# Kernel optimization log

Hardware: AMD Instinct MI355X
Metric: run time of the kernel (lower is better)

The kernel has to match this reference:

```python
import jax, jax.numpy as jnp
import numpy as np

EPS = 1e-5  # BatchNorm2d default eps


def _conv3x3(x, w):
    # x: [B,C,H,W], w: [O,I,3,3], stride 1, padding 1, no bias
    return jax.lax.conv_general_dilated(
        x, w, window_strides=(1, 1), padding=((1, 1), (1, 1)),
        dimension_numbers=("NCHW", "OIHW", "NCHW"))


def setup_inputs() -> dict:
    key = jax.random.key(0)
    k1, k2, k3 = jax.random.split(key, 3)
    B, C, H, W = 4, 64, 24, 24
    x = jax.random.normal(k1, (B, C, H, W), dtype=jnp.float32)
    gamma = jnp.ones((C,), dtype=jnp.float32)
    beta = jnp.zeros((C,), dtype=jnp.float32)
    # fan-based init scale as in the custom Conv2d (scale=1 and scale=1e-6)
    fan_qkv = (C + 3 * C) / 2 * 9
    bound_qkv = np.sqrt(3.0 / fan_qkv)
    w_qkv = jax.random.uniform(k2, (3 * C, C, 3, 3), minval=-bound_qkv,
                               maxval=bound_qkv, dtype=jnp.float32)
    fan_out = (C + C) / 2 * 9
    bound_out = np.sqrt(3.0 * 1e-6 / fan_out)
    w_out = jax.random.uniform(k3, (C, C, 3, 3), minval=-bound_out,
                               maxval=bound_out, dtype=jnp.float32)
    return {"x": x, "gamma": gamma, "beta": beta, "w_qkv": w_qkv, "w_out": w_out}


def reference(x, gamma, beta, w_qkv, w_out):
    B, C, H, W = x.shape
    # BatchNorm2d (training-mode batch statistics, biased variance)
    mean = jnp.mean(x, axis=(0, 2, 3), keepdims=True)
    var = jnp.var(x, axis=(0, 2, 3), keepdims=True)
    xn = (x - mean) * jax.lax.rsqrt(var + EPS)
    xn = xn * gamma[None, :, None, None] + beta[None, :, None, None]
    qkv = _conv3x3(xn, w_qkv)            # [B,3C,H,W]
    q, k, v = jnp.split(qkv, 3, axis=1)  # each [B,C,H,W]
    scale = 1.0 / np.sqrt(C)
    # per-channel attention: head_dim=1, heads=C
    logits = jnp.einsum("bcyx,bchw->bcyxhw", q, k) * scale  # [B,C,H,W,H,W]
    attn = jax.nn.softmax(logits.reshape(B, C, H, W, H * W), axis=-1)
    attn = attn.reshape(B, C, H, W, H, W)
    out_v = jnp.einsum("bcyxhw,bchw->bcyx", attn, v)  # [B,C,H,W]
    return x + _conv3x3(out_v, w_out)
```

## Files before the change

kernel.cpp:

```cpp
#include <hip/hip_runtime.h>
#include <math.h>

#define B_SZ 4
#define C_IN 64
#define HW_ 576
#define PPLANE 728
#define XH_N   (B_SZ * 32 * PPLANE)
#define WQH_N  (192 * 32 * 9)
#define WOH_N  (64 * 32 * 9)

typedef _Float16 h2 __attribute__((ext_vector_type(2)));
typedef _Float16 h4 __attribute__((ext_vector_type(4)));
typedef _Float16 h8 __attribute__((ext_vector_type(8)));

static __device__ __forceinline__ h2 lo2(h4 v) { return __builtin_shufflevector(v, v, 0, 1); }
static __device__ __forceinline__ h2 hi2(h4 v) { return __builtin_shufflevector(v, v, 2, 3); }

static __device__ __forceinline__ float dot2(h2 a, h2 b, float c) {
#if __has_builtin(__builtin_amdgcn_fdot2)
  return __builtin_amdgcn_fdot2(a, b, c, false);
#else
  return c + (float)a.x * (float)b.x + (float)a.y * (float)b.y;
#endif
}

static __device__ __forceinline__ float frcp(float d) {
#if __has_builtin(__builtin_amdgcn_rcpf)
  return __builtin_amdgcn_rcpf(d);
#else
  return 1.0f / d;
#endif
}

__global__ __launch_bounds__(256)
void stats_pack_kernel(const float* __restrict__ x, const float* __restrict__ gamma,
                       const float* __restrict__ beta, const float* __restrict__ wq,
                       const float* __restrict__ wo, h2* __restrict__ xh,
                       h2* __restrict__ wqh, h2* __restrict__ woh) {
  const int bid = blockIdx.x, tid = threadIdx.x;
  if (bid < 128) {
    const int icp = bid & 31, b = bid >> 5;
    __shared__ float rs[4], rss[4], ab[4];
    const int c = icp * 2 + (tid >> 7);
    float s = 0.f, ss = 0.f;
    for (int i = (tid & 127); i < B_SZ * HW_; i += 128) {
      int b2 = i / HW_, px = i - b2 * HW_;
      float v = x[(b2 * C_IN + c) * HW_ + px];
      s += v; ss = fmaf(v, v, ss);
    }
#pragma unroll
    for (int off = 32; off > 0; off >>= 1) {
      s += __shfl_down(s, off); ss += __shfl_down(ss, off);
    }
    if ((tid & 63) == 0) { rs[tid >> 6] = s; rss[tid >> 6] = ss; }
    __syncthreads();
    if (tid < 2) {
      float S = rs[tid * 2] + rs[tid * 2 + 1], SS = rss[tid * 2] + rss[tid * 2 + 1];
      const float inv_n = 1.f / (B_SZ * HW_);
      float mean = S * inv_n;
      float var  = SS * inv_n - mean * mean;
      float a = rsqrtf(var + 1e-5f) * gamma[icp * 2 + tid];
      ab[tid * 2] = a;
      ab[tid * 2 + 1] = fmaf(-mean, a, beta[icp * 2 + tid]);
    }
    __syncthreads();
    const float a0 = ab[0], b0 = ab[1], a1 = ab[2], b1 = ab[3];
    h2* plane = xh + (size_t)(b * 32 + icp) * PPLANE;
    const float* src0 = x + (size_t)(b * C_IN + icp * 2) * HW_;
    for (int e = tid; e < PPLANE; e += 256) {
      int rrow = e / 28, ecol = e - rrow * 28;
      int yy = rrow - 1, xx = ecol - 1;
      float f0 = 0.f, f1 = 0.f;
      if ((unsigned)yy < 24u && (unsigned)xx < 24u) {
        f0 = fmaf(src0[yy * 24 + xx],       a0, b0);
        f1 = fmaf(src0[HW_ + yy * 24 + xx], a1, b1);
      }
      h2 v; v.x = (_Float16)f0; v.y = (_Float16)f1;
      plane[e] = v;
    }
  } else {
    const int base = (bid - 128) * 576;
    for (int t = base + tid; t < base + 576; t += 256) {
      if (t < WQH_N) {
        int tt = t % 9; int r = t / 9;
        int o = r % 3; r /= 3;
        int icp = r % 32; int g = r / 32;
        int oc = g + 64 * o, ic = icp * 2;
        h2 v;
        v.x = (_Float16)wq[(oc * C_IN + ic) * 9 + tt];
        v.y = (_Float16)wq[(oc * C_IN + ic + 1) * 9 + tt];
        wqh[t] = v;
      } else {
        int t0 = t - WQH_N;
        int tt = t0 % 9; int r = t0 / 9;
        int icp = r % 32; int oc = r / 32;
        int ic = icp * 2;
        h2 v;
        v.x = (_Float16)(wo[(oc * C_IN + ic) * 9 + tt] * 4096.f);
        v.y = (_Float16)(wo[(oc * C_IN + ic + 1) * 9 + tt] * 4096.f);
        woh[t0] = v;
      }
    }
  }
}

__global__ __launch_bounds__(576)
void qkv_attn_kernel(const h2* __restrict__ xh, const h2* __restrict__ wqh,
                     h2* __restrict__ outv) {
  const int bid = blockIdx.x, tid = threadIdx.x;
  const int b = bid >> 6, c = bid & 63;
  const int sub = tid / 288;
  const int r = tid - sub * 288;
  const int y = r / 12, x0 = (r % 12) * 2;

  __shared__ __align__(16) char smem[26080];
  h2*    Wl  = (h2*)smem;
  float* cb  = (float*)smem;
  float2* kvs = (float2*)(smem + 6912);
  float* qs  = (float*)(smem + 11520);
  float* red = (float*)(smem + 13824);
  float* FGf = (float*)(smem + 14472);
  float* red2 = (float*)(smem + 14560);

  for (int j = tid; j < 864; j += 576) {
    int icp = j / 27, rem = j - icp * 27;
    Wl[icp * 32 + rem] = wqh[c * 864 + j];
  }
  __syncthreads();

  float acc[3][2] = {{0.f, 0.f}, {0.f, 0.f}, {0.f, 0.f}};
  const int icp0 = sub * 16;
  const int yo = y * 28 + x0;
  const h2* dbase = xh + ((size_t)(b * 32 + icp0) * PPLANE + yo);
#pragma unroll
  for (int i = 0; i < 16; ++i) {
    const h2* dp = dbase + (size_t)i * PPLANE;
    h4 r0a = *(const h4*)(dp);      h4 r0b = *(const h4*)(dp + 2);
    h4 r1a = *(const h4*)(dp + 28); h4 r1b = *(const h4*)(dp + 30);
    h4 r2a = *(const h4*)(dp + 56); h4 r2b = *(const h4*)(dp + 58);
    const h2* wrow = Wl + (icp0 + i) * 32;
    union { h8 v8[7]; h2 v2[28]; } W;
#pragma unroll
    for (int j8 = 0; j8 < 7; ++j8) W.v8[j8] = *(const h8*)(wrow + j8 * 4);
#pragma unroll
    for (int o = 0; o < 3; ++o) {
      float a0 = acc[o][0], a1 = acc[o][1];
      a0 = dot2(lo2(r0a), W.v2[o * 9 + 0], a0);  a1 = dot2(hi2(r0a), W.v2[o * 9 + 0], a1);
      a0 = dot2(hi2(r0a), W.v2[o * 9 + 1], a0);  a1 = dot2(lo2(r0b), W.v2[o * 9 + 1], a1);
      a0 = dot2(lo2(r0b), W.v2[o * 9 + 2], a0);  a1 = dot2(hi2(r0b), W.v2[o * 9 + 2], a1);
      a0 = dot2(lo2(r1a), W.v2[o * 9 + 3], a0);  a1 = dot2(hi2(r1a), W.v2[o * 9 + 3], a1);
      a0 = dot2(hi2(r1a), W.v2[o * 9 + 4], a0);  a1 = dot2(lo2(r1b), W.v2[o * 9 + 4], a1);
      a0 = dot2(lo2(r1b), W.v2[o * 9 + 5], a0);  a1 = dot2(hi2(r1b), W.v2[o * 9 + 5], a1);
      a0 = dot2(lo2(r2a), W.v2[o * 9 + 6], a0);  a1 = dot2(hi2(r2a), W.v2[o * 9 + 6], a1);
      a0 = dot2(hi2(r2a), W.v2[o * 9 + 7], a0);  a1 = dot2(lo2(r2b), W.v2[o * 9 + 7], a1);
      a0 = dot2(lo2(r2b), W.v2[o * 9 + 8], a0);  a1 = dot2(hi2(r2b), W.v2[o * 9 + 8], a1);
      acc[o][0] = a0; acc[o][1] = a1;
    }
  }
  __syncthreads();
  if (sub == 1) {
#pragma unroll
    for (int o = 0; o < 3; ++o) {
      cb[(o * 288 + r) * 2 + 0] = acc[o][0];
      cb[(o * 288 + r) * 2 + 1] = acc[o][1];
    }
  }
  __syncthreads();
  const float scale_l2e = 0.125f * 1.44269504088896341f;
  if (sub == 0) {
    float q0 = acc[0][0] + cb[(0 * 288 + r) * 2 + 0];
    float q1 = acc[0][1] + cb[(0 * 288 + r) * 2 + 1];
    float k0 = acc[1][0] + cb[(1 * 288 + r) * 2 + 0];
    float k1 = acc[1][1] + cb[(1 * 288 + r) * 2 + 1];
    float v0 = acc[2][0] + cb[(2 * 288 + r) * 2 + 0];
    float v1 = acc[2][1] + cb[(2 * 288 + r) * 2 + 1];
    qs[2 * r] = q0 * scale_l2e; qs[2 * r + 1] = q1 * scale_l2e;
    kvs[2 * r] = make_float2(k0, v0);
    kvs[2 * r + 1] = make_float2(k1, v1);
  }
  __syncthreads();

  const float s = qs[tid];
  float smax = s, smin = s;
#pragma unroll
  for (int off = 32; off > 0; off >>= 1) {
    smax = fmaxf(smax, __shfl_down(smax, off));
    smin = fminf(smin, __shfl_down(smin, off));
  }
  const int wid = tid >> 6;
  if ((tid & 63) == 0) { red[wid] = smax; red[10 + wid] = smin; }
  __syncthreads();
  smax = red[0]; smin = red[10];
#pragma unroll
  for (int w = 1; w < 9; ++w) {
    smax = fmaxf(smax, red[w]); smin = fminf(smin, red[10 + w]);
  }
  const float cc = 0.5f * (smax + smin);
  const float rr = fmaxf(0.5f * (smax - smin), 1e-6f);
  const float COS[9] = { 0.98480775f,  0.86602540f,  0.64278761f,  0.34202014f, 0.f,
                        -0.34202014f, -0.64278761f, -0.86602540f, -0.98480775f };
  const float WJ[9]  = { 0.17364818f, -0.5f,  0.76604444f, -0.93969262f, 1.f,
                        -0.93969262f, 0.76604444f, -0.5f, 0.17364818f };
  float xj[9];
#pragma unroll
  for (int j = 0; j < 9; ++j) xj[j] = fmaf(rr, COS[j], cc);

  const float kk = kvs[tid].x, vv = kvs[tid].y;
  float fj[9], gj[9];
#pragma unroll
  for (int j = 0; j < 9; ++j) {
    float E = __builtin_amdgcn_exp2f(xj[j] * kk);
    gj[j] = E; fj[j] = E * vv;
  }
#pragma unroll
  for (int j = 0; j < 9; ++j) {
    fj[j] += __shfl_xor(fj[j], 1); gj[j] += __shfl_xor(gj[j], 1);
    fj[j] += __shfl_xor(fj[j], 2); gj[j] += __shfl_xor(gj[j], 2);
  }
  if ((tid & 3) == 0) {
    const int row = tid >> 2;
#pragma unroll
    for (int j = 0; j < 9; ++j) {
      red2[row * 20 + j] = fj[j];
      red2[row * 20 + 9 + j] = gj[j];
    }
  }
  __syncthreads();
  if (tid < 144) {
    const int j = tid >> 3, chunk = tid & 7;
    float sum = 0.f;
#pragma unroll
    for (int i = 0; i < 18; ++i) sum += red2[(chunk + 8 * i) * 20 + j];
    sum += __shfl_xor(sum, 1);
    sum += __shfl_xor(sum, 2);
    sum += __shfl_xor(sum, 4);
    if (chunk == 0) FGf[j] = sum;
  }
  __syncthreads();

  float num = 0.f, den = 0.f;
#pragma unroll
  for (int j = 0; j < 9; ++j) {
    float d = s - xj[j];
    d = copysignf(fmaxf(fabsf(d), 1e-7f), d);
    float mu = WJ[j] * frcp(d);
    num = fmaf(mu, FGf[j], num);
    den = fmaf(mu, FGf[9 + j], den);
  }
  float outval = num / den;

  const int icp = c >> 1, hc = c & 1;
  _Float16* plane = reinterpret_cast<_Float16*>(outv + ((size_t)(b * 32) + icp) * PPLANE);
  const int yy = tid / 24, xx = tid - yy * 24;
  plane[((yy + 1) * 28 + (xx + 1)) * 2 + hc] = (_Float16)outval;
  if (tid < 100) {
    int rrow, e;
    if (tid < 26)      { rrow = 0;            e = tid; }
    else if (tid < 52) { rrow = 25;           e = tid - 26; }
    else if (tid < 76) { rrow = tid - 52 + 1; e = 0; }
    else               { rrow = tid - 76 + 1; e = 25; }
    plane[(rrow * 28 + e) * 2 + hc] = (_Float16)0.f;
  }
}

__global__ __launch_bounds__(576)
void conv_out_kernel(const h2* __restrict__ outv, const h2* __restrict__ woh,
                     const float* __restrict__ x, float* __restrict__ out) {
  const int bid = blockIdx.x, tid = threadIdx.x;
  const int b = bid >> 6, oc = bid & 63;
  const int sub = tid / 288;
  const int r = tid - sub * 288;
  const int y = r / 12, x0 = (r % 12) * 2;
  __shared__ __align__(16) char smem[4096];

  h2* Wl = (h2*)smem;
  for (int j = tid; j < 288; j += 576) {
    int icp = j / 9, rem = j - icp * 9;
    Wl[icp * 16 + rem] = woh[oc * 288 + j];
  }
  __syncthreads();

  float a0 = 0.f, a1 = 0.f;
  const int icp0 = sub * 16;
  const int yo = y * 28 + x0;
  const h2* dbase = outv + ((size_t)(b * 32 + icp0) * PPLANE + yo);
#pragma unroll
  for (int i = 0; i < 16; ++i) {
    const h2* dp = dbase + (size_t)i * PPLANE;
    h4 r0a = *(const h4*)(dp);      h4 r0b = *(const h4*)(dp + 2);
    h4 r1a = *(const h4*)(dp + 28); h4 r1b = *(const h4*)(dp + 30);
    h4 r2a = *(const h4*)(dp + 56); h4 r2b = *(const h4*)(dp + 58);
    const h2* wrow = Wl + (icp0 + i) * 16;
    union { h8 v8[3]; h2 v2[12]; } W;
    W.v8[0] = *(const h8*)(wrow);
    W.v8[1] = *(const h8*)(wrow + 4);
    W.v8[2] = *(const h8*)(wrow + 8);
    a0 = dot2(lo2(r0a), W.v2[0], a0);  a1 = dot2(hi2(r0a), W.v2[0], a1);
    a0 = dot2(hi2(r0a), W.v2[1], a0);  a1 = dot2(lo2(r0b), W.v2[1], a1);
    a0 = dot2(lo2(r0b), W.v2[2], a0);  a1 = dot2(hi2(r0b), W.v2[2], a1);
    a0 = dot2(lo2(r1a), W.v2[3], a0);  a1 = dot2(hi2(r1a), W.v2[3], a1);
    a0 = dot2(hi2(r1a), W.v2[4], a0);  a1 = dot2(lo2(r1b), W.v2[4], a1);
    a0 = dot2(lo2(r1b), W.v2[5], a0);  a1 = dot2(hi2(r1b), W.v2[5], a1);
    a0 = dot2(lo2(r2a), W.v2[6], a0);  a1 = dot2(hi2(r2a), W.v2[6], a1);
    a0 = dot2(hi2(r2a), W.v2[7], a0);  a1 = dot2(lo2(r2b), W.v2[7], a1);
    a0 = dot2(lo2(r2b), W.v2[8], a0);  a1 = dot2(hi2(r2b), W.v2[8], a1);
  }
  __syncthreads();
  float* cb = (float*)smem;
  if (sub == 1) { cb[r * 2] = a0; cb[r * 2 + 1] = a1; }
  __syncthreads();
  if (sub == 0) {
    size_t idx = ((size_t)(b * C_IN + oc) * HW_) + y * 24 + x0;
    float2 xr = *reinterpret_cast<const float2*>(x + idx);
    const float inv = 1.f / 4096.f;
    float2 v;
    v.x = fmaf(a0 + cb[r * 2],     inv, xr.x);
    v.y = fmaf(a1 + cb[r * 2 + 1], inv, xr.y);
    *reinterpret_cast<float2*>(out + idx) = v;
  }
}

extern "C" void kernel_launch(void* const* d_in, const int* in_sizes, int n_in,
                              void* d_out, int out_size, void* d_ws, size_t ws_size,
                              hipStream_t stream) {
  const float* x     = (const float*)d_in[0];
  const float* gamma = (const float*)d_in[1];
  const float* beta  = (const float*)d_in[2];
  const float* w_qkv = (const float*)d_in[3];
  const float* w_out = (const float*)d_in[4];
  float* out = (float*)d_out;

  h2* xh   = (h2*)d_ws;
  h2* wqh  = xh + XH_N;
  h2* woh  = wqh + WQH_N;
  h2* outv = woh + WOH_N;

  stats_pack_kernel<<<256, 256, 0, stream>>>(x, gamma, beta, w_qkv, w_out, xh, wqh, woh);
  qkv_attn_kernel<<<256, 576, 0, stream>>>(xh, wqh, outv);
  conv_out_kernel<<<256, 576, 0, stream>>>(outv, woh, x, out);
}
```

Measured before the change: 26.08 us.

## Fuse weight packing into conv kernels and compute 4 pixels per thread with 4-way channel split

Weight conversion to packed fp16 moves out of the stats kernel and into the two conv kernels, which now read the fp32 weights directly. The stats kernel launches only the 128 normalisation blocks. Both convolutions switch from 2 pixels per thread over 2 channel groups to 4 pixels per thread over 4 channel groups, using wider h8 loads so each loaded row segment is reused across more outputs. The partial sums are reduced through a larger shared buffer. This cuts redundant input loads and removes the separate packing work, at the cost of more shared memory, an extra reduction step and repeated weight conversion in every block.

```diff
diff --git a/kernel.cpp b/kernel.cpp
--- a/kernel.cpp
+++ b/kernel.cpp
@@ -6,15 +6,9 @@
 #define HW_ 576
 #define PPLANE 728
 #define XH_N   (B_SZ * 32 * PPLANE)
-#define WQH_N  (192 * 32 * 9)
-#define WOH_N  (64 * 32 * 9)
 
 typedef _Float16 h2 __attribute__((ext_vector_type(2)));
-typedef _Float16 h4 __attribute__((ext_vector_type(4)));
 typedef _Float16 h8 __attribute__((ext_vector_type(8)));
-
-static __device__ __forceinline__ h2 lo2(h4 v) { return __builtin_shufflevector(v, v, 0, 1); }
-static __device__ __forceinline__ h2 hi2(h4 v) { return __builtin_shufflevector(v, v, 2, 3); }
 
 static __device__ __forceinline__ float dot2(h2 a, h2 b, float c) {
 #if __has_builtin(__builtin_amdgcn_fdot2)
@@ -34,149 +28,133 @@
 
 __global__ __launch_bounds__(256)
 void stats_pack_kernel(const float* __restrict__ x, const float* __restrict__ gamma,
-                       const float* __restrict__ beta, const float* __restrict__ wq,
-                       const float* __restrict__ wo, h2* __restrict__ xh,
-                       h2* __restrict__ wqh, h2* __restrict__ woh) {
+                       const float* __restrict__ beta, h2* __restrict__ xh) {
   const int bid = blockIdx.x, tid = threadIdx.x;
-  if (bid < 128) {
-    const int icp = bid & 31, b = bid >> 5;
-    __shared__ float rs[4], rss[4], ab[4];
-    const int c = icp * 2 + (tid >> 7);
-    float s = 0.f, ss = 0.f;
-    for (int i = (tid & 127); i < B_SZ * HW_; i += 128) {
-      int b2 = i / HW_, px = i - b2 * HW_;
-      float v = x[(b2 * C_IN + c) * HW_ + px];
-      s += v; ss = fmaf(v, v, ss);
-    }
-#pragma unroll
-    for (int off = 32; off > 0; off >>= 1) {
-      s += __shfl_down(s, off); ss += __shfl_down(ss, off);
-    }
-    if ((tid & 63) == 0) { rs[tid >> 6] = s; rss[tid >> 6] = ss; }
-    __syncthreads();
-    if (tid < 2) {
-      float S = rs[tid * 2] + rs[tid * 2 + 1], SS = rss[tid * 2] + rss[tid * 2 + 1];
-      const float inv_n = 1.f / (B_SZ * HW_);
-      float mean = S * inv_n;
-      float var  = SS * inv_n - mean * mean;
-      float a = rsqrtf(var + 1e-5f) * gamma[icp * 2 + tid];
-      ab[tid * 2] = a;
-      ab[tid * 2 + 1] = fmaf(-mean, a, beta[icp * 2 + tid]);
-    }
-    __syncthreads();
-    const float a0 = ab[0], b0 = ab[1], a1 = ab[2], b1 = ab[3];
-    h2* plane = xh + (size_t)(b * 32 + icp) * PPLANE;
-    const float* src0 = x + (size_t)(b * C_IN + icp * 2) * HW_;
-    for (int e = tid; e < PPLANE; e += 256) {
-      int rrow = e / 28, ecol = e - rrow * 28;
-      int yy = rrow - 1, xx = ecol - 1;
-      float f0 = 0.f, f1 = 0.f;
-      if ((unsigned)yy < 24u && (unsigned)xx < 24u) {
-        f0 = fmaf(src0[yy * 24 + xx],       a0, b0);
-        f1 = fmaf(src0[HW_ + yy * 24 + xx], a1, b1);
-      }
-      h2 v; v.x = (_Float16)f0; v.y = (_Float16)f1;
-      plane[e] = v;
-    }
-  } else {
-    const int base = (bid - 128) * 576;
-    for (int t = base + tid; t < base + 576; t += 256) {
-      if (t < WQH_N) {
-        int tt = t % 9; int r = t / 9;
-        int o = r % 3; r /= 3;
-        int icp = r % 32; int g = r / 32;
-        int oc = g + 64 * o, ic = icp * 2;
-        h2 v;
-        v.x = (_Float16)wq[(oc * C_IN + ic) * 9 + tt];
-        v.y = (_Float16)wq[(oc * C_IN + ic + 1) * 9 + tt];
-        wqh[t] = v;
-      } else {
-        int t0 = t - WQH_N;
-        int tt = t0 % 9; int r = t0 / 9;
-        int icp = r % 32; int oc = r / 32;
-        int ic = icp * 2;
-        h2 v;
-        v.x = (_Float16)(wo[(oc * C_IN + ic) * 9 + tt] * 4096.f);
-        v.y = (_Float16)(wo[(oc * C_IN + ic + 1) * 9 + tt] * 4096.f);
-        woh[t0] = v;
-      }
-    }
+  const int icp = bid & 31, b = bid >> 5;
+  __shared__ float rs[4], rss[4], ab[4];
+  const int c = icp * 2 + (tid >> 7);
+  float s = 0.f, ss = 0.f;
+  for (int i = (tid & 127); i < B_SZ * HW_; i += 128) {
+    int b2 = i / HW_, px = i - b2 * HW_;
+    float v = x[(b2 * C_IN + c) * HW_ + px];
+    s += v; ss = fmaf(v, v, ss);
+  }
+#pragma unroll
+  for (int off = 32; off > 0; off >>= 1) {
+    s += __shfl_down(s, off); ss += __shfl_down(ss, off);
+  }
+  if ((tid & 63) == 0) { rs[tid >> 6] = s; rss[tid >> 6] = ss; }
+  __syncthreads();
+  if (tid < 2) {
+    float S = rs[tid * 2] + rs[tid * 2 + 1], SS = rss[tid * 2] + rss[tid * 2 + 1];
+    const float inv_n = 1.f / (B_SZ * HW_);
+    float mean = S * inv_n;
+    float var  = SS * inv_n - mean * mean;
+    float a = rsqrtf(var + 1e-5f) * gamma[icp * 2 + tid];
+    ab[tid * 2] = a;
+    ab[tid * 2 + 1] = fmaf(-mean, a, beta[icp * 2 + tid]);
+  }
+  __syncthreads();
+  const float a0 = ab[0], b0 = ab[1], a1 = ab[2], b1 = ab[3];
+  h2* plane = xh + (size_t)(b * 32 + icp) * PPLANE;
+  const float* src0 = x + (size_t)(b * C_IN + icp * 2) * HW_;
+  for (int e = tid; e < PPLANE; e += 256) {
+    int rrow = e / 28, ecol = e - rrow * 28;
+    int yy = rrow - 1, xx = ecol - 1;
+    float f0 = 0.f, f1 = 0.f;
+    if ((unsigned)yy < 24u && (unsigned)xx < 24u) {
+      f0 = fmaf(src0[yy * 24 + xx],       a0, b0);
+      f1 = fmaf(src0[HW_ + yy * 24 + xx], a1, b1);
+    }
+    h2 v; v.x = (_Float16)f0; v.y = (_Float16)f1;
+    plane[e] = v;
   }
 }
 
 __global__ __launch_bounds__(576)
-void qkv_attn_kernel(const h2* __restrict__ xh, const h2* __restrict__ wqh,
+void qkv_attn_kernel(const h2* __restrict__ xh, const float* __restrict__ wq,
                      h2* __restrict__ outv) {
   const int bid = blockIdx.x, tid = threadIdx.x;
   const int b = bid >> 6, c = bid & 63;
-  const int sub = tid / 288;
-  const int r = tid - sub * 288;
-  const int y = r / 12, x0 = (r % 12) * 2;
-
-  __shared__ __align__(16) char smem[26080];
+  const int sub = tid / 144;
+  const int r = tid - sub * 144;
+  const int y = r / 6, x0 = (r % 6) * 4;
+
+  __shared__ __align__(16) char smem[43424];
   h2*    Wl  = (h2*)smem;
-  float* cb  = (float*)smem;
-  float2* kvs = (float2*)(smem + 6912);
-  float* qs  = (float*)(smem + 11520);
-  float* red = (float*)(smem + 13824);
-  float* FGf = (float*)(smem + 14472);
-  float* red2 = (float*)(smem + 14560);
+  float* cb  = (float*)(smem + 4096);
+  float2* kvs = (float2*)(smem + 24832);
+  float* qs  = (float*)(smem + 29440);
+  float* red = (float*)(smem + 31744);
+  float* FGf = (float*)(smem + 31824);
+  float* red2 = (float*)(smem + 31904);
 
   for (int j = tid; j < 864; j += 576) {
     int icp = j / 27, rem = j - icp * 27;
-    Wl[icp * 32 + rem] = wqh[c * 864 + j];
-  }
-  __syncthreads();
-
-  float acc[3][2] = {{0.f, 0.f}, {0.f, 0.f}, {0.f, 0.f}};
-  const int icp0 = sub * 16;
-  const int yo = y * 28 + x0;
-  const h2* dbase = xh + ((size_t)(b * 32 + icp0) * PPLANE + yo);
-#pragma unroll
-  for (int i = 0; i < 16; ++i) {
-    const h2* dp = dbase + (size_t)i * PPLANE;
-    h4 r0a = *(const h4*)(dp);      h4 r0b = *(const h4*)(dp + 2);
-    h4 r1a = *(const h4*)(dp + 28); h4 r1b = *(const h4*)(dp + 30);
-    h4 r2a = *(const h4*)(dp + 56); h4 r2b = *(const h4*)(dp + 58);
+    int o = rem / 9, t = rem - o * 9;
+    int oc = c + 64 * o;
+    h2 v;
+    v.x = (_Float16)wq[(oc * C_IN + 2 * icp) * 9 + t];
+    v.y = (_Float16)wq[(oc * C_IN + 2 * icp + 1) * 9 + t];
+    Wl[icp * 32 + rem] = v;
+  }
+  __syncthreads();
+
+  float acc[3][4] = {{0.f,0.f,0.f,0.f},{0.f,0.f,0.f,0.f},{0.f,0.f,0.f,0.f}};
+  const int icp0 = sub * 8;
+  const h2* dbase = xh + ((size_t)(b * 32 + icp0) * PPLANE + y * 28 + x0);
+#pragma unroll
+  for (int i = 0; i < 8; ++i) {
+    const h2* dp = dbase + i * PPLANE;
+    union { h8 v8[2]; h2 v2[8]; } R0, R1, R2;
+    R0.v8[0] = *(const h8*)(dp);      R0.v8[1] = *(const h8*)(dp + 4);
+    R1.v8[0] = *(const h8*)(dp + 28); R1.v8[1] = *(const h8*)(dp + 32);
+    R2.v8[0] = *(const h8*)(dp + 56); R2.v8[1] = *(const h8*)(dp + 60);
     const h2* wrow = Wl + (icp0 + i) * 32;
     union { h8 v8[7]; h2 v2[28]; } W;
 #pragma unroll
     for (int j8 = 0; j8 < 7; ++j8) W.v8[j8] = *(const h8*)(wrow + j8 * 4);
 #pragma unroll
     for (int o = 0; o < 3; ++o) {
-      float a0 = acc[o][0], a1 = acc[o][1];
-      a0 = dot2(lo2(r0a), W.v2[o * 9 + 0], a0);  a1 = dot2(hi2(r0a), W.v2[o * 9 + 0], a1);
-      a0 = dot2(hi2(r0a), W.v2[o * 9 + 1], a0);  a1 = dot2(lo2(r0b), W.v2[o * 9 + 1], a1);
-      a0 = dot2(lo2(r0b), W.v2[o * 9 + 2], a0);  a1 = dot2(hi2(r0b), W.v2[o * 9 + 2], a1);
-      a0 = dot2(lo2(r1a), W.v2[o * 9 + 3], a0);  a1 = dot2(hi2(r1a), W.v2[o * 9 + 3], a1);
-      a0 = dot2(hi2(r1a), W.v2[o * 9 + 4], a0);  a1 = dot2(lo2(r1b), W.v2[o * 9 + 4], a1);
-      a0 = dot2(lo2(r1b), W.v2[o * 9 + 5], a0);  a1 = dot2(hi2(r1b), W.v2[o * 9 + 5], a1);
-      a0 = dot2(lo2(r2a), W.v2[o * 9 + 6], a0);  a1 = dot2(hi2(r2a), W.v2[o * 9 + 6], a1);
-      a0 = dot2(hi2(r2a), W.v2[o * 9 + 7], a0);  a1 = dot2(lo2(r2b), W.v2[o * 9 + 7], a1);
-      a0 = dot2(lo2(r2b), W.v2[o * 9 + 8], a0);  a1 = dot2(hi2(r2b), W.v2[o * 9 + 8], a1);
-      acc[o][0] = a0; acc[o][1] = a1;
-    }
-  }
-  __syncthreads();
-  if (sub == 1) {
-#pragma unroll
-    for (int o = 0; o < 3; ++o) {
-      cb[(o * 288 + r) * 2 + 0] = acc[o][0];
-      cb[(o * 288 + r) * 2 + 1] = acc[o][1];
-    }
+#pragma unroll
+      for (int p = 0; p < 4; ++p) {
+        float a = acc[o][p];
+        a = dot2(R0.v2[p + 0], W.v2[o * 9 + 0], a);
+        a = dot2(R0.v2[p + 1], W.v2[o * 9 + 1], a);
+        a = dot2(R0.v2[p + 2], W.v2[o * 9 + 2], a);
+        a = dot2(R1.v2[p + 0], W.v2[o * 9 + 3], a);
+        a = dot2(R1.v2[p + 1], W.v2[o * 9 + 4], a);
+        a = dot2(R1.v2[p + 2], W.v2[o * 9 + 5], a);
+        a = dot2(R2.v2[p + 0], W.v2[o * 9 + 6], a);
+        a = dot2(R2.v2[p + 1], W.v2[o * 9 + 7], a);
+        a = dot2(R2.v2[p + 2], W.v2[o * 9 + 8], a);
+        acc[o][p] = a;
+      }
+    }
+  }
+  __syncthreads();
+  if (sub != 0) {
+    const int base = (sub - 1) * 3 * 576;
+#pragma unroll
+    for (int o = 0; o < 3; ++o)
+#pragma unroll
+      for (int p = 0; p < 4; ++p)
+        cb[base + o * 576 + r * 4 + p] = acc[o][p];
   }
   __syncthreads();
   const float scale_l2e = 0.125f * 1.44269504088896341f;
   if (sub == 0) {
-    float q0 = acc[0][0] + cb[(0 * 288 + r) * 2 + 0];
-    float q1 = acc[0][1] + cb[(0 * 288 + r) * 2 + 1];
-    float k0 = acc[1][0] + cb[(1 * 288 + r) * 2 + 0];
-    float k1 = acc[1][1] + cb[(1 * 288 + r) * 2 + 1];
-    float v0 = acc[2][0] + cb[(2 * 288 + r) * 2 + 0];
-    float v1 = acc[2][1] + cb[(2 * 288 + r) * 2 + 1];
-    qs[2 * r] = q0 * scale_l2e; qs[2 * r + 1] = q1 * scale_l2e;
-    kvs[2 * r] = make_float2(k0, v0);
-    kvs[2 * r + 1] = make_float2(k1, v1);
+#pragma unroll
+    for (int p = 0; p < 4; ++p) {
+      float qv = acc[0][p] + cb[0 * 576 + r * 4 + p]
+               + cb[3 * 576 + r * 4 + p] + cb[6 * 576 + r * 4 + p];
+      float kv = acc[1][p] + cb[1 * 576 + r * 4 + p]
+               + cb[4 * 576 + r * 4 + p] + cb[7 * 576 + r * 4 + p];
+      float vv = acc[2][p] + cb[2 * 576 + r * 4 + p]
+               + cb[5 * 576 + r * 4 + p] + cb[8 * 576 + r * 4 + p];
+      qs[4 * r + p] = qv * scale_l2e;
+      kvs[4 * r + p] = make_float2(kv, vv);
+    }
   }
   __syncthreads();
 
@@ -264,59 +242,74 @@
 }
 
 __global__ __launch_bounds__(576)
-void conv_out_kernel(const h2* __restrict__ outv, const h2* __restrict__ woh,
+void conv_out_kernel(const h2* __restrict__ outv, const float* __restrict__ wo,
                      const float* __restrict__ x, float* __restrict__ out) {
   const int bid = blockIdx.x, tid = threadIdx.x;
   const int b = bid >> 6, oc = bid & 63;
-  const int sub = tid / 288;
-  const int r = tid - sub * 288;
-  const int y = r / 12, x0 = (r % 12) * 2;
-  __shared__ __align__(16) char smem[4096];
-
-  h2* Wl = (h2*)smem;
+  const int sub = tid / 144;
+  const int r = tid - sub * 144;
+  const int y = r / 6, x0 = (r % 6) * 4;
+
+  __shared__ __align__(16) char smem[8960];
+  h2*    Wl = (h2*)smem;
+  float* cb = (float*)(smem + 2048);
+
   for (int j = tid; j < 288; j += 576) {
-    int icp = j / 9, rem = j - icp * 9;
-    Wl[icp * 16 + rem] = woh[oc * 288 + j];
-  }
-  __syncthreads();
-
-  float a0 = 0.f, a1 = 0.f;
-  const int icp0 = sub * 16;
-  const int yo = y * 28 + x0;
-  const h2* dbase = outv + ((size_t)(b * 32 + icp0) * PPLANE + yo);
-#pragma unroll
-  for (int i = 0; i < 16; ++i) {
-    const h2* dp = dbase + (size_t)i * PPLANE;
-    h4 r0a = *(const h4*)(dp);      h4 r0b = *(const h4*)(dp + 2);
-    h4 r1a = *(const h4*)(dp + 28); h4 r1b = *(const h4*)(dp + 30);
-    h4 r2a = *(const h4*)(dp + 56); h4 r2b = *(const h4*)(dp + 58);
+    int icp = j / 9, t = j - icp * 9;
+    h2 v;
+    v.x = (_Float16)(wo[(oc * C_IN + 2 * icp) * 9 + t] * 4096.f);
+    v.y = (_Float16)(wo[(oc * C_IN + 2 * icp + 1) * 9 + t] * 4096.f);
+    Wl[icp * 16 + t] = v;
+  }
+  __syncthreads();
+
+  float acc[4] = {0.f, 0.f, 0.f, 0.f};
+  const int icp0 = sub * 8;
+  const h2* dbase = outv + ((size_t)(b * 32 + icp0) * PPLANE + y * 28 + x0);
+#pragma unroll
+  for (int i = 0; i < 8; ++i) {
+    const h2* dp = dbase + i * PPLANE;
+    union { h8 v8[2]; h2 v2[8]; } R0, R1, R2;
+    R0.v8[0] = *(const h8*)(dp);      R0.v8[1] = *(const h8*)(dp + 4);
+    R1.v8[0] = *(const h8*)(dp + 28); R1.v8[1] = *(const h8*)(dp + 32);
+    R2.v8[0] = *(const h8*)(dp + 56); R2.v8[1] = *(const h8*)(dp + 60);
     const h2* wrow = Wl + (icp0 + i) * 16;
     union { h8 v8[3]; h2 v2[12]; } W;
     W.v8[0] = *(const h8*)(wrow);
     W.v8[1] = *(const h8*)(wrow + 4);
     W.v8[2] = *(const h8*)(wrow + 8);
-    a0 = dot2(lo2(r0a), W.v2[0], a0);  a1 = dot2(hi2(r0a), W.v2[0], a1);
-    a0 = dot2(hi2(r0a), W.v2[1], a0);  a1 = dot2(lo2(r0b), W.v2[1], a1);
-    a0 = dot2(lo2(r0b), W.v2[2], a0);  a1 = dot2(hi2(r0b), W.v2[2], a1);
-    a0 = dot2(lo2(r1a), W.v2[3], a0);  a1 = dot2(hi2(r1a), W.v2[3], a1);
-    a0 = dot2(hi2(r1a), W.v2[4], a0);  a1 = dot2(lo2(r1b), W.v2[4], a1);
-    a0 = dot2(lo2(r1b), W.v2[5], a0);  a1 = dot2(hi2(r1b), W.v2[5], a1);
-    a0 = dot2(lo2(r2a), W.v2[6], a0);  a1 = dot2(hi2(r2a), W.v2[6], a1);
-    a0 = dot2(hi2(r2a), W.v2[7], a0);  a1 = dot2(lo2(r2b), W.v2[7], a1);
-    a0 = dot2(lo2(r2b), W.v2[8], a0);  a1 = dot2(hi2(r2b), W.v2[8], a1);
-  }
-  __syncthreads();
-  float* cb = (float*)smem;
-  if (sub == 1) { cb[r * 2] = a0; cb[r * 2 + 1] = a1; }
+#pragma unroll
+    for (int p = 0; p < 4; ++p) {
+      float a = acc[p];
+      a = dot2(R0.v2[p + 0], W.v2[0], a);
+      a = dot2(R0.v2[p + 1], W.v2[1], a);
+      a = dot2(R0.v2[p + 2], W.v2[2], a);
+      a = dot2(R1.v2[p + 0], W.v2[3], a);
+      a = dot2(R1.v2[p + 1], W.v2[4], a);
+      a = dot2(R1.v2[p + 2], W.v2[5], a);
+      a = dot2(R2.v2[p + 0], W.v2[6], a);
+      a = dot2(R2.v2[p + 1], W.v2[7], a);
+      a = dot2(R2.v2[p + 2], W.v2[8], a);
+      acc[p] = a;
+    }
+  }
+  __syncthreads();
+  if (sub != 0) {
+    const int base = ((sub - 1) * 144 + r) * 4;
+#pragma unroll
+    for (int p = 0; p < 4; ++p) cb[base + p] = acc[p];
+  }
   __syncthreads();
   if (sub == 0) {
-    size_t idx = ((size_t)(b * C_IN + oc) * HW_) + y * 24 + x0;
-    float2 xr = *reinterpret_cast<const float2*>(x + idx);
+    size_t idx = ((size_t)(b * C_IN + oc) * HW_) + 4 * r;
+    float4 xr = *reinterpret_cast<const float4*>(x + idx);
     const float inv = 1.f / 4096.f;
-    float2 v;
-    v.x = fmaf(a0 + cb[r * 2],     inv, xr.x);
-    v.y = fmaf(a1 + cb[r * 2 + 1], inv, xr.y);
-    *reinterpret_cast<float2*>(out + idx) = v;
+    float4 v;
+    v.x = fmaf(acc[0] + cb[(0 * 144 + r) * 4 + 0] + cb[(1 * 144 + r) * 4 + 0] + cb[(2 * 144 + r) * 4 + 0], inv, xr.x);
+    v.y = fmaf(acc[1] + cb[(0 * 144 + r) * 4 + 1] + cb[(1 * 144 + r) * 4 + 1] + cb[(2 * 144 + r) * 4 + 1], inv, xr.y);
+    v.z = fmaf(acc[2] + cb[(0 * 144 + r) * 4 + 2] + cb[(1 * 144 + r) * 4 + 2] + cb[(2 * 144 + r) * 4 + 2], inv, xr.z);
+    v.w = fmaf(acc[3] + cb[(0 * 144 + r) * 4 + 3] + cb[(1 * 144 + r) * 4 + 3] + cb[(2 * 144 + r) * 4 + 3], inv, xr.w);
+    *reinterpret_cast<float4*>(out + idx) = v;
   }
 }
 
@@ -331,11 +324,9 @@
   float* out = (float*)d_out;
 
   h2* xh   = (h2*)d_ws;
-  h2* wqh  = xh + XH_N;
-  h2* woh  = wqh + WQH_N;
-  h2* outv = woh + WOH_N;
-
-  stats_pack_kernel<<<256, 256, 0, stream>>>(x, gamma, beta, w_qkv, w_out, xh, wqh, woh);
-  qkv_attn_kernel<<<256, 576, 0, stream>>>(xh, wqh, outv);
-  conv_out_kernel<<<256, 576, 0, stream>>>(outv, woh, x, out);
-}
+  h2* outv = xh + XH_N;
+
+  stats_pack_kernel<<<128, 256, 0, stream>>>(x, gamma, beta, xh);
+  qkv_attn_kernel<<<256, 576, 0, stream>>>(xh, w_qkv, outv);
+  conv_out_kernel<<<256, 576, 0, stream>>>(outv, w_out, x, out);
+}
```

Measured after the change: 26.45 us. Within noise of the previous version (+1.4%).
